# Kernel optimization log

Hardware: AMD Instinct MI355X
Metric: run time of the kernel (lower is better)

Reference implementation:

```python
import jax, jax.numpy as jnp
import numpy as np

B, L, C, Y, DIM = 64, 64, 4, 0, 2  # batch, lattice size, n_colors, tau-shift, shift axis


def _coloring_probes():
    # k x k block coloring for C colors (C must be a perfect square here; C=4 -> k=2)
    k = int(round(np.sqrt(C)))
    i = np.arange(L)[:, None]
    j = np.arange(L)[None, :]
    col = (i % k) * k + (j % k)  # (L, L) color index per site
    probes = (col[None, :, :] == np.arange(C)[:, None, None]).astype(np.float32)
    return jnp.asarray(probes)  # (C, L, L) one-hot color masks


def _gelu(x):
    return jax.nn.gelu(x, approximate=False)  # torch nn.GELU default = exact erf


def _forward(x, sW1, sb1, sW2, sb2, sW3, sb3, aW1, ab1, aW2, ab2):
    # site features: phi, 2D lattice laplacian (periodic), phi_{x+tau}, phi_{x-tau}
    lap = (jnp.roll(x, 1, 1) + jnp.roll(x, -1, 1)
           + jnp.roll(x, 1, 2) + jnp.roll(x, -1, 2) - 4.0 * x)
    phi_tau = jnp.roll(x, -Y, axis=DIM)
    phi_mtau = jnp.roll(x, Y, axis=DIM)
    f = jnp.stack([x, lap, phi_tau, phi_mtau], axis=-1)  # (B, L, L, 4)
    h = _gelu(f @ sW1 + sb1)
    h = _gelu(h @ sW2 + sb2)
    h = (h @ sW3 + sb3)[..., 0]                          # (B, L, L)
    h_mean = h.mean(axis=(1, 2))
    h_var = jnp.var(h, axis=(1, 2), ddof=1)              # torch .var() is unbiased
    h_sq_mean = (h * h).mean(axis=(1, 2))
    a = jnp.stack([h_mean, h_var, h_sq_mean], axis=1)    # (B, 3)
    a = _gelu(a @ aW1 + ab1)
    return (a @ aW2 + ab2)[..., 0]                       # (B,)


def setup_inputs() -> dict:
    key = jax.random.key(0)
    ks = jax.random.split(key, 8)

    def w(k, shape, fan_in):
        return jax.random.normal(k, shape, jnp.float32) / np.sqrt(fan_in).astype(np.float32)

    return {
        "x": jax.random.normal(ks[0], (B, L, L), jnp.float32),
        "signs": jax.random.randint(ks[1], (C, B, L, L), 0, 2, jnp.int32),
        "site_W1": w(ks[2], (4, 128), 4),
        "site_b1": jnp.zeros((128,), jnp.float32),
        "site_W2": w(ks[3], (128, 128), 128),
        "site_b2": jnp.zeros((128,), jnp.float32),
        "site_W3": w(ks[4], (128, 1), 128),
        "site_b3": jnp.zeros((1,), jnp.float32),
        "agg_W1": w(ks[5], (3, 64), 3),
        "agg_b1": jnp.zeros((64,), jnp.float32),
        "agg_W2": w(ks[6], (64, 1), 64),
        "agg_b2": jnp.zeros((1,), jnp.float32),
    }


def reference(x, signs, site_W1, site_b1, site_W2, site_b2, site_W3, site_b3,
              agg_W1, agg_b1, agg_W2, agg_b2):
    params = (site_W1, site_b1, site_W2, site_b2, site_W3, site_b3,
              agg_W1, agg_b1, agg_W2, agg_b2)
    fsum = lambda xx: _forward(xx, *params).sum()  # batches are independent, so sum is safe

    # first-order gradient grad_x F, shape (B, L, L)
    grad = jax.grad(fsum)(x)

    # probing laplacian with coloring + Rademacher signs, batched over colors
    probes = _coloring_probes()                                   # (C, L, L)
    z = (2.0 * signs.astype(jnp.float32) - 1.0) * probes[:, None]  # (C, B, L, L)
    # hvp_c = H @ z_c via forward-over-reverse AD (replaces per-color autograd.grad loop)
    hvp = jax.vmap(lambda zc: jax.jvp(jax.grad(fsum), (x,), (zc,))[1])(z)  # (C, B, L, L)
    lapl = jnp.sum(hvp * z, axis=(0, 2, 3))                       # (B,)

    # pack (grad, lapl) into one array: (B, L*L + 1)
    return jnp.concatenate([grad.reshape(B, -1), lapl[:, None]], axis=1)
```

## Files before the change

### kernel.cpp

```cpp
#include <hip/hip_runtime.h>
#include <hip/hip_bf16.h>
#include <math.h>

typedef unsigned short ushort_t;
typedef unsigned int   u32;
typedef __attribute__((ext_vector_type(8))) short s8v;
typedef __attribute__((ext_vector_type(4))) float f4v;
typedef __attribute__((ext_vector_type(2))) float f2v;

#define LL 64
#define NB 64
#define NSITE 4096
#define BN 262144
#define RED_OFF 0
#define WA_OFF  11264
#define WB_OFF  11392
#define PL_OFF  12288
#define BF_OFF  (PL_OFF + 6*BN)

#if __has_builtin(__builtin_amdgcn_exp2f)
#define EXP2F(x) __builtin_amdgcn_exp2f(x)
#else
#define EXP2F(x) __expf(0.6931471805599453f*(x))
#endif

__device__ __forceinline__ void gelu3(float u, float &h, float &d, float &e){
  float E   = __expf(-0.5f * u * u);
  float phi = 0.3989422804014327f * E;
  float az  = fabsf(u) * 0.70710678118654752f;
  float t   = __builtin_amdgcn_rcpf(1.0f + 0.3275911f * az);
  float p   = t*(0.254829592f + t*(-0.284496736f + t*(1.421413741f + t*(-1.453152027f + t*1.061405429f))));
  float erfabs = 1.0f - p * E;
  float erfv   = __builtin_copysignf(erfabs, u);
  float Phi = 0.5f * (1.0f + erfv);
  h = u * Phi;
  d = Phi + u * phi;
  e = phi * (2.0f - u * u);
}

__device__ __forceinline__ void gelu3x2(f2v u, f2v &h, f2v &d, f2v &e){
  f2v u2 = u * u;
  f2v m  = u2 * (-0.72134752044448170368f);
  f2v E;  E.x = EXP2F(m.x); E.y = EXP2F(m.y);
  f2v phi = 0.3989422804014327f * E;
  f2v az;
  az.x = fabsf(u.x) * 0.70710678118654752f;
  az.y = fabsf(u.y) * 0.70710678118654752f;
  f2v den = 0.3275911f * az + 1.0f;
  f2v t;  t.x = __builtin_amdgcn_rcpf(den.x); t.y = __builtin_amdgcn_rcpf(den.y);
  f2v p = t*(0.254829592f + t*(-0.284496736f + t*(1.421413741f + t*(-1.453152027f + t*1.061405429f))));
  f2v erfabs = 1.0f - p * E;
  f2v erfv;
  erfv.x = __builtin_copysignf(erfabs.x, u.x);
  erfv.y = __builtin_copysignf(erfabs.y, u.y);
  f2v Phi = 0.5f * erfv + 0.5f;
  h = u * Phi;
  d = u * phi + Phi;
  e = phi * (2.0f - u2);
}

#define DPP_ADD(v, ctrl) { \
  int _si = __builtin_amdgcn_update_dpp(0, __builtin_bit_cast(int, v), ctrl, 0xf, 0xf, true); \
  v += __builtin_bit_cast(float, _si); }

__device__ __forceinline__ float redjb16(float v){
  DPP_ADD(v, 0xB1);
  DPP_ADD(v, 0x4E);
  DPP_ADD(v, 0x124);
  DPP_ADD(v, 0x128);
  return v;
}
__device__ __forceinline__ float red64(float v){
  v = redjb16(v);
  v += __shfl_xor(v, 16);
  v += __shfl_xor(v, 32);
  return v;
}

__device__ __forceinline__ ushort_t bf16rne(float v){
  union { float f; u32 i; } x; x.f = v;
  u32 r = x.i + 0x7FFFu + ((x.i >> 16) & 1u);
  return (ushort_t)(r >> 16);
}
__device__ __forceinline__ u32 pkbf(float a, float b){
  __hip_bfloat162 t = __float22bfloat162_rn(make_float2(a, b));
  u32 r;
  __builtin_memcpy(&r, &t, sizeof(r));
  return r;
}
__device__ __forceinline__ u32 pkbf2(f2v v){
  return pkbf(v.x, v.y);
}

__global__ __launch_bounds__(256, 4) void k_pre(
    const float* __restrict__ W1g, const float* __restrict__ W2g,
    float* __restrict__ ws, float* __restrict__ out)
{
  int t = blockIdx.x * 256 + threadIdx.x;
  if (blockIdx.x == 0 && threadIdx.x < 128) {
    int k = threadIdx.x;
    ws[WA_OFF + k] = W1g[k] + W1g[256+k] + W1g[384+k];
    ws[WB_OFF + k] = W1g[128+k];
  }
  if (blockIdx.x == 1 && threadIdx.x < 64) {
    out[(size_t)threadIdx.x*4097 + 4096] = 0.f;
  }
  short* BF = (short*)(ws + BF_OFF);
  int w = t >> 9, nt = (t >> 8) & 1, kt = (t >> 6) & 3, lane = t & 63;
  int q = lane >> 4, nlo = lane & 15;
  int n = w*32 + nt*16 + nlo;
  s8v vh;
  #pragma unroll
  for (int jj = 0; jj < 8; ++jj) {
    int k = kt*32 + q*8 + jj;
    vh[jj] = (short)bf16rne(W2g[k*128 + n]);
  }
  *(s8v*)&BF[t*8] = vh;
}

__global__ __launch_bounds__(256, 3) void k_c1(
    const float* __restrict__ xg, const int* __restrict__ signs,
    const float* __restrict__ b1g, const float* __restrict__ b2g,
    const float* __restrict__ W3g, const float* __restrict__ b3g,
    float* __restrict__ ws)
{
  __shared__ alignas(16) short AF[12288];
  __shared__ float xS[6][64];
  __shared__ char  zS[6][64];
  __shared__ float EP[16][7][4];

  const int tid  = threadIdx.x;
  const int lane = tid & 63;
  const int w    = tid >> 6;
  const int rg4  = (lane >> 4) << 2;

  const int blk = blockIdx.x;
  const int b   = blk >> 4;
  const int i0  = (blk & 15) << 2;

  const s8v* BhT = (const s8v*)((const short*)(ws + BF_OFF)) + (w*512 + lane);

  float4 b2H[2], w3H[2];
  #pragma unroll
  for (int nt = 0; nt < 2; ++nt) {
    int n0 = w*32 + nt*16 + rg4;
    b2H[nt] = *(const float4*)(b2g + n0);
    w3H[nt] = *(const float4*)(W3g + n0);
  }
  float b3v = b3g[0];

  const int s_  = tid & 15;
  const int ko_ = tid >> 4;
  float4 waH[2], wbH[2], b1H[2];
  #pragma unroll
  for (int half = 0; half < 2; ++half) {
    int k0 = ko_*8 + half*4;
    waH[half] = *(const float4*)(ws + WA_OFF + k0);
    wbH[half] = *(const float4*)(ws + WB_OFF + k0);
    b1H[half] = *(const float4*)(b1g + k0);
  }

  for (int t = tid; t < 384; t += 256) {
    int r = t >> 6, j = t & 63;
    int gr = (i0 - 1 + r) & 63;
    xS[r][j] = xg[(size_t)b*NSITE + gr*64 + j];
    int c = ((gr & 1) << 1) | (j & 1);
    zS[r][j] = (char)(2*signs[((c*NB + b)*LL + gr)*LL + j] - 1);
  }
  __syncthreads();

  float racc[10];
  #pragma unroll
  for (int n = 0; n < 10; ++n) racc[n] = 0.f;

  const f4v Zf = {0.f, 0.f, 0.f, 0.f};

  #pragma unroll 1
  for (int ch = 0; ch < 16; ++ch) {
    const int lr = 1 + (ch >> 2);
    const int jb = ch & 3;
    const int i  = i0 + (ch >> 2);

    s8v pb00 = BhT[0],  pb10 = BhT[256];
    s8v pb01 = BhT[64], pb11 = BhT[320];

    {
      int j = jb*16 + s_, jm = (j+63)&63, jp = (j+1)&63;
      float p = xS[lr][j];
      float l = xS[lr-1][j] + xS[lr+1][j] + xS[lr][jm] + xS[lr][jp] - 4.0f*p;
      u32 vv[6][4];
      #pragma unroll
      for (int half = 0; half < 2; ++half) {
        const float* waA = (const float*)&waH[half];
        const float* wbA = (const float*)&wbH[half];
        const float* b1A = (const float*)&b1H[half];
        #pragma unroll
        for (int pr = 0; pr < 2; ++pr) {
          f2v wa = {waA[pr*2], waA[pr*2+1]};
          f2v wb = {wbA[pr*2], wbA[pr*2+1]};
          f2v bb = {b1A[pr*2], b1A[pr*2+1]};
          f2v u = p*wa + l*wb + bb;
          f2v h, dd, ee;
          gelu3x2(u, h, dd, ee);
          int c = half*2 + pr;
          vv[0][c] = pkbf2(h);
          vv[1][c] = pkbf2(dd*wa);
          vv[2][c] = pkbf2(dd*wb);
          f2v ea = ee*wa, eb = ee*wb;
          vv[3][c] = pkbf2(ea*wa);
          vv[4][c] = pkbf2(ea*wb);
          vv[5][c] = pkbf2(eb*wb);
        }
      }
      short* base = &AF[(ko_>>2)*3072 + ((ko_&3)*16 + s_)*8];
      #pragma unroll
      for (int pp = 0; pp < 6; ++pp)
        *(int4*)&base[pp*512] = make_int4((int)vv[pp][0], (int)vv[pp][1],
                                          (int)vv[pp][2], (int)vv[pp][3]);
    }
    __syncthreads();

    f4v acc[6][2];
    __builtin_amdgcn_s_setprio(1);
    {
      const short* base = &AF[lane*8];
      #pragma unroll
      for (int pp = 0; pp < 6; ++pp) {
        s8v ah = *(const s8v*)&base[pp*512];
        acc[pp][0] = __builtin_amdgcn_mfma_f32_16x16x32_bf16(pb00, ah, Zf, 0, 0, 0);
        acc[pp][1] = __builtin_amdgcn_mfma_f32_16x16x32_bf16(pb10, ah, Zf, 0, 0, 0);
      }
    }
    s8v bh0 = pb01, bh1 = pb11;
    #pragma unroll 1
    for (int kt = 1; kt < 4; ++kt) {
      s8v nh0 = bh0, nh1 = bh1;
      if (kt != 3) {
        int o = (kt + 1) * 64;
        nh0 = BhT[o]; nh1 = BhT[256 + o];
      }
      const short* base = &AF[kt*3072 + lane*8];
      #pragma unroll
      for (int pp = 0; pp < 6; ++pp) {
        s8v ah = *(const s8v*)&base[pp*512];
        acc[pp][0] = __builtin_amdgcn_mfma_f32_16x16x32_bf16(bh0, ah, acc[pp][0], 0, 0, 0);
        acc[pp][1] = __builtin_amdgcn_mfma_f32_16x16x32_bf16(bh1, ah, acc[pp][1], 0, 0, 0);
      }
      bh0 = nh0; bh1 = nh1;
    }
    __builtin_amdgcn_s_setprio(0);

    {
      f2v qh = {0.f,0.f}, qA = {0.f,0.f}, qB = {0.f,0.f};
      f2v qa = {0.f,0.f}, qb = {0.f,0.f}, qc = {0.f,0.f};
      #pragma unroll
      for (int nt = 0; nt < 2; ++nt) {
        const float* b2A = (const float*)&b2H[nt];
        const float* w3A = (const float*)&w3H[nt];
        #pragma unroll
        for (int pr = 0; pr < 2; ++pr) {
          const int r0 = pr*2;
          f2v uu  = (f2v){acc[0][nt][r0], acc[0][nt][r0+1]}
                  + (f2v){b2A[r0], b2A[r0+1]};
          f2v w3p = {w3A[r0], w3A[r0+1]};
          f2v h2, d2, e2;
          gelu3x2(uu, h2, d2, e2);
          f2v wd = w3p*d2, we = w3p*e2;
          f2v A  = {acc[1][nt][r0], acc[1][nt][r0+1]};
          f2v Bv = {acc[2][nt][r0], acc[2][nt][r0+1]};
          f2v t3 = {acc[3][nt][r0], acc[3][nt][r0+1]};
          f2v t4 = {acc[4][nt][r0], acc[4][nt][r0+1]};
          f2v t5 = {acc[5][nt][r0], acc[5][nt][r0+1]};
          qh += w3p*h2;
          qA += wd*A;
          qB += wd*Bv;
          qa += we*(A*A)   + wd*t3;
          qb += we*(A*Bv)  + wd*t4;
          qc += we*(Bv*Bv) + wd*t5;
        }
      }
      float sh = qh.x + qh.y;
      float sA = qA.x + qA.y;
      float sB = qB.x + qB.y;
      float sa = qa.x + qa.y;
      float sb = qb.x + qb.y;
      float sc = qc.x + qc.y;
      sh += __shfl_xor(sh, 16); sh += __shfl_xor(sh, 32);
      sA += __shfl_xor(sA, 16); sA += __shfl_xor(sA, 32);
      sB += __shfl_xor(sB, 16); sB += __shfl_xor(sB, 32);
      sa += __shfl_xor(sa, 16); sa += __shfl_xor(sa, 32);
      sb += __shfl_xor(sb, 16); sb += __shfl_xor(sb, 32);
      sc += __shfl_xor(sc, 16); sc += __shfl_xor(sc, 32);
      if (lane < 16) {
        EP[lane][0][w] = sh;
        EP[lane][1][w] = sA;
        EP[lane][2][w] = sB;
        EP[lane][3][w] = sa;
        EP[lane][4][w] = sb;
        EP[lane][5][w] = sc;
      }
    }
    __syncthreads();

    if (tid < 16) {
      int s = tid;
      float h = 0.f, RA = 0.f, RB = 0.f, TAa = 0.f, TAb = 0.f, TBb = 0.f;
      #pragma unroll
      for (int ww = 0; ww < 4; ++ww) {
        h   += EP[s][0][ww];
        RA  += EP[s][1][ww];
        RB  += EP[s][2][ww];
        TAa += EP[s][3][ww];
        TAb += EP[s][4][ww];
        TBb += EP[s][5][ww];
      }
      h += b3v;
      float* P = ws + PL_OFF;
      int j = jb*16 + s;
      size_t site = (size_t)b*NSITE + i*64 + j;
      P[0*BN + site] = h;
      P[1*BN + site] = RA;
      P[2*BN + site] = RB;
      P[3*BN + site] = TAa;
      P[4*BN + site] = TAb;
      P[5*BN + site] = TBb;

      int jm = (j+63)&63, jp = (j+1)&63;
      int c0 = ((i & 1) << 1) | (j & 1);
      float hd[4] = {0.f, 0.f, 0.f, 0.f};
      hd[c0]     = (float)zS[lr][j] * (RA - 4.0f*RB);
      hd[c0 ^ 1] = (float)(zS[lr][jm] + zS[lr][jp]) * RB;
      hd[c0 ^ 2] = (float)(zS[lr-1][j] + zS[lr+1][j]) * RB;
      racc[0] += h;
      racc[1] += h*h;
      #pragma unroll
      for (int cc = 0; cc < 4; ++cc) {
        racc[2+cc] += hd[cc];
        racc[6+cc] += h*hd[cc];
      }
    }
  }

  if (tid < 16) {
    #pragma unroll
    for (int n = 0; n < 10; ++n) racc[n] = redjb16(racc[n]);
    if (tid == 0) {
      #pragma unroll
      for (int n = 0; n < 10; ++n) ws[RED_OFF + blk*10 + n] = racc[n];
    }
  }
}

__global__ __launch_bounds__(256, 4) void k_c2(
    const int* __restrict__ signs,
    const float* __restrict__ aW1g, const float* __restrict__ ab1g,
    const float* __restrict__ aW2g,
    float* __restrict__ ws, float* __restrict__ out)
{
  __shared__ float part[4];
  __shared__ float coefL[10];
  __shared__ float redS[10];
  __shared__ float cbS[6][64];
  int blk = blockIdx.x;
  int b = blk >> 4, rg = blk & 15;
  int tid = threadIdx.x;

  if (tid < 160) {
    int qq = tid >> 4, g = tid & 15;
    float v = ws[RED_OFF + (b*16 + g)*10 + qq];
    v = redjb16(v);
    if (g == 0) redS[qq] = v;
  }
  __syncthreads();

  if (tid < 64) {
    int k = tid;
    const float Nf = 4096.0f, Nm1 = 4095.0f;
    float S1 = redS[0], S2 = redS[1];
    float m = S1/Nf, q = S2/Nf;
    float v = (S2 - S1*S1/Nf)/Nm1;
    float w0 = aW1g[k], w1 = aW1g[64+k], w2 = aW1g[128+k];
    float t = m*w0 + v*w1 + q*w2 + ab1g[k];
    float gh, gd, ge;
    gelu3(t, gh, gd, ge);
    float o = aW2g[k];
    float g1o = gd*o, g2o = ge*o;
    float da0 = w0*g1o, da1 = w1*g1o, da2 = w2*g1o;
    float M00 = w0*w0*g2o, M01 = w0*w1*g2o, M02 = w0*w2*g2o;
    float M11 = w1*w1*g2o, M12 = w1*w2*g2o, M22 = w2*w2*g2o;
    da0 = red64(da0); da1 = red64(da1); da2 = red64(da2);
    M00 = red64(M00); M01 = red64(M01); M02 = red64(M02);
    M11 = red64(M11); M12 = red64(M12); M22 = red64(M22);
    if (k == 0) {
      coefL[0] = da0/Nf - 2.0f*da1*m/Nm1;
      coefL[1] = 2.0f*da1/Nm1 + 2.0f*da2/Nf;
      #pragma unroll
      for (int c = 0; c < 4; ++c) {
        float s1 = redS[2 + c], s2 = redS[6 + c];
        float md = s1/Nf, qd = 2.0f*s2/Nf;
        float vd = (2.0f*s2 - 2.0f*S1*s1/Nf)/Nm1;
        float dd0 = M00*md + M01*vd + M02*qd;
        float dd1 = M01*md + M11*vd + M12*qd;
        float dd2 = M02*md + M12*vd + M22*qd;
        coefL[2+c] = dd0/Nf - 2.0f*(dd1*m + da1*md)/Nm1;
        coefL[6+c] = 2.0f*dd1/Nm1 + 2.0f*dd2/Nf;
      }
    }
  }
  __syncthreads();

  const float* P = ws + PL_OFF;
  int base = b*NSITE;
  float alpha = coefL[0], beta = coefL[1];

  for (int t = tid; t < 384; t += 256) {
    int r = t >> 6, jj = t & 63;
    int gr = (rg*4 - 1 + r) & 63;
    int sidx = base + gr*64 + jj;
    cbS[r][jj] = (alpha + beta*P[sidx]) * P[2*BN + sidx];
  }
  __syncthreads();

  int rl = tid >> 6, j = tid & 63;
  int i = rg*4 + rl;
  int im=(i+63)&63, ip=(i+1)&63, jm=(j+63)&63, jp=(j+1)&63;
  int s  = base + i*64 + j;
  float h  = P[s], RA = P[BN+s], RB = P[2*BN+s];
  float TAa= P[3*BN+s], TAb = P[4*BN+s], TBb = P[5*BN+s];
  float g  = alpha + beta*h;
  int lr2 = rl + 1;
  float cb  = cbS[lr2][j];
  float cbu = cbS[lr2-1][j], cbd = cbS[lr2+1][j];
  float cbl = cbS[lr2][jm],  cbr = cbS[lr2][jp];
  float grad = g*RA + (cbu + cbd + cbl + cbr - 4.0f*cb);
  out[(size_t)b*4097 + i*64 + j] = grad;

  int c0 = ((i & 1) << 1) | (j & 1);
  int c1 = c0 ^ 1, c2 = c0 ^ 2;
  float zv = 2.0f*(float)signs[((c0*NB + b)*LL + i )*LL + j ] - 1.0f;
  float zl = 2.0f*(float)signs[((c1*NB + b)*LL + i )*LL + jm] - 1.0f;
  float zr = 2.0f*(float)signs[((c1*NB + b)*LL + i )*LL + jp] - 1.0f;
  float zu = 2.0f*(float)signs[((c2*NB + b)*LL + im)*LL + j ] - 1.0f;
  float zd = 2.0f*(float)signs[((c2*NB + b)*LL + ip)*LL + j ] - 1.0f;
  float sjr = zl + zr, sud = zu + zd;
  float hd0 = zv*(RA - 4.0f*RB);
  float hd1 = sjr*RB, hd2 = sud*RB;
  float gd0 = coefL[2+c0] + coefL[6+c0]*h + beta*hd0;
  float gd1 = coefL[2+c1] + coefL[6+c1]*h + beta*hd1;
  float gd2 = coefL[2+c2] + coefL[6+c2]*h + beta*hd2;
  float ca0 = gd0*RA + g*( zv*TAa - 4.0f*zv*TAb );
  float cb0 = gd0*RB + g*( zv*TAb - 4.0f*zv*TBb );
  float cb1 = gd1*RB + g*( sjr*TBb );
  float cb2 = gd2*RB + g*( sud*TBb );
  float contrib = zv*ca0 - 4.0f*zv*cb0 + sjr*cb1 + sud*cb2;

  float vsum = red64(contrib);
  int wv = tid >> 6;
  if ((tid & 63) == 0) part[wv] = vsum;
  __syncthreads();
  if (tid == 0)
    atomicAdd(out + (size_t)b*4097 + 4096,
              part[0] + part[1] + part[2] + part[3]);
}

extern "C" void kernel_launch(void* const* d_in, const int* in_sizes, int n_in,
                              void* d_out, int out_size, void* d_ws, size_t ws_size,
                              hipStream_t stream) {
  const float* xg    = (const float*)d_in[0];
  const int*   signs = (const int*)d_in[1];
  const float* W1    = (const float*)d_in[2];
  const float* b1    = (const float*)d_in[3];
  const float* W2    = (const float*)d_in[4];
  const float* b2    = (const float*)d_in[5];
  const float* W3    = (const float*)d_in[6];
  const float* b3    = (const float*)d_in[7];
  const float* aW1   = (const float*)d_in[8];
  const float* ab1   = (const float*)d_in[9];
  const float* aW2   = (const float*)d_in[10];
  float* ws  = (float*)d_ws;
  float* out = (float*)d_out;

  hipLaunchKernelGGL(k_pre, dim3(8),    dim3(256), 0, stream, W1, W2, ws, out);
  hipLaunchKernelGGL(k_c1,  dim3(1024), dim3(256), 0, stream,
                     xg, signs, b1, b2, W3, b3, ws);
  hipLaunchKernelGGL(k_c2,  dim3(1024), dim3(256), 0, stream,
                     signs, aW1, ab1, aW2, ws, out);
}
```

Baseline: 181.2 us.

## Fuse second pass into main kernel via last-block-per-batch atomic ticket

Removes the separate k_c2 launch. Each k_c1 block increments a per-batch counter after writing its partial reductions, and the last of the 16 blocks for a batch runs the aggregation and writes the whole 4096-site gradient and Laplacian. This saves one kernel launch and the global sync between kernels, and drops the output atomicAdd. In exchange the per-batch epilogue is serialized on one block (64 blocks doing 4096 sites each) instead of spread over 1024 blocks, which can leave a long tail.

```diff
diff --git a/kernel.cpp b/kernel.cpp
--- a/kernel.cpp
+++ b/kernel.cpp
@@ -13,6 +13,7 @@
 #define NSITE 4096
 #define BN 262144
 #define RED_OFF 0
+#define CNT_OFF 10240
 #define WA_OFF  11264
 #define WB_OFF  11392
 #define PL_OFF  12288
@@ -94,7 +95,7 @@
 
 __global__ __launch_bounds__(256, 4) void k_pre(
     const float* __restrict__ W1g, const float* __restrict__ W2g,
-    float* __restrict__ ws, float* __restrict__ out)
+    float* __restrict__ ws)
 {
   int t = blockIdx.x * 256 + threadIdx.x;
   if (blockIdx.x == 0 && threadIdx.x < 128) {
@@ -103,7 +104,7 @@
     ws[WB_OFF + k] = W1g[128+k];
   }
   if (blockIdx.x == 1 && threadIdx.x < 64) {
-    out[(size_t)threadIdx.x*4097 + 4096] = 0.f;
+    ((int*)ws)[CNT_OFF + threadIdx.x] = 0;
   }
   short* BF = (short*)(ws + BF_OFF);
   int w = t >> 9, nt = (t >> 8) & 1, kt = (t >> 6) & 3, lane = t & 63;
@@ -122,12 +123,18 @@
     const float* __restrict__ xg, const int* __restrict__ signs,
     const float* __restrict__ b1g, const float* __restrict__ b2g,
     const float* __restrict__ W3g, const float* __restrict__ b3g,
-    float* __restrict__ ws)
+    const float* __restrict__ aW1g, const float* __restrict__ ab1g,
+    const float* __restrict__ aW2g,
+    float* __restrict__ ws, float* __restrict__ out)
 {
   __shared__ alignas(16) short AF[12288];
   __shared__ float xS[6][64];
   __shared__ char  zS[6][64];
   __shared__ float EP[16][7][4];
+  __shared__ float coefL[10];
+  __shared__ float redS[10];
+  __shared__ float partS[4];
+  __shared__ int   tickS;
 
   const int tid  = threadIdx.x;
   const int lane = tid & 63;
@@ -349,21 +356,13 @@
       for (int n = 0; n < 10; ++n) ws[RED_OFF + blk*10 + n] = racc[n];
     }
   }
-}
-
-__global__ __launch_bounds__(256, 4) void k_c2(
-    const int* __restrict__ signs,
-    const float* __restrict__ aW1g, const float* __restrict__ ab1g,
-    const float* __restrict__ aW2g,
-    float* __restrict__ ws, float* __restrict__ out)
-{
-  __shared__ float part[4];
-  __shared__ float coefL[10];
-  __shared__ float redS[10];
-  __shared__ float cbS[6][64];
-  int blk = blockIdx.x;
-  int b = blk >> 4, rg = blk & 15;
-  int tid = threadIdx.x;
+
+  __threadfence();
+  __syncthreads();
+  if (tid == 0) tickS = atomicAdd(((int*)ws) + CNT_OFF + b, 1);
+  __syncthreads();
+  if (tickS != 15) return;
+  __threadfence();
 
   if (tid < 160) {
     int qq = tid >> 4, g = tid & 15;
@@ -410,57 +409,56 @@
   __syncthreads();
 
   const float* P = ws + PL_OFF;
-  int base = b*NSITE;
-  float alpha = coefL[0], beta = coefL[1];
-
-  for (int t = tid; t < 384; t += 256) {
-    int r = t >> 6, jj = t & 63;
-    int gr = (rg*4 - 1 + r) & 63;
-    int sidx = base + gr*64 + jj;
-    cbS[r][jj] = (alpha + beta*P[sidx]) * P[2*BN + sidx];
-  }
-  __syncthreads();
-
-  int rl = tid >> 6, j = tid & 63;
-  int i = rg*4 + rl;
-  int im=(i+63)&63, ip=(i+1)&63, jm=(j+63)&63, jp=(j+1)&63;
-  int s  = base + i*64 + j;
-  float h  = P[s], RA = P[BN+s], RB = P[2*BN+s];
-  float TAa= P[3*BN+s], TAb = P[4*BN+s], TBb = P[5*BN+s];
-  float g  = alpha + beta*h;
-  int lr2 = rl + 1;
-  float cb  = cbS[lr2][j];
-  float cbu = cbS[lr2-1][j], cbd = cbS[lr2+1][j];
-  float cbl = cbS[lr2][jm],  cbr = cbS[lr2][jp];
-  float grad = g*RA + (cbu + cbd + cbl + cbr - 4.0f*cb);
-  out[(size_t)b*4097 + i*64 + j] = grad;
-
-  int c0 = ((i & 1) << 1) | (j & 1);
-  int c1 = c0 ^ 1, c2 = c0 ^ 2;
-  float zv = 2.0f*(float)signs[((c0*NB + b)*LL + i )*LL + j ] - 1.0f;
-  float zl = 2.0f*(float)signs[((c1*NB + b)*LL + i )*LL + jm] - 1.0f;
-  float zr = 2.0f*(float)signs[((c1*NB + b)*LL + i )*LL + jp] - 1.0f;
-  float zu = 2.0f*(float)signs[((c2*NB + b)*LL + im)*LL + j ] - 1.0f;
-  float zd = 2.0f*(float)signs[((c2*NB + b)*LL + ip)*LL + j ] - 1.0f;
-  float sjr = zl + zr, sud = zu + zd;
-  float hd0 = zv*(RA - 4.0f*RB);
-  float hd1 = sjr*RB, hd2 = sud*RB;
-  float gd0 = coefL[2+c0] + coefL[6+c0]*h + beta*hd0;
-  float gd1 = coefL[2+c1] + coefL[6+c1]*h + beta*hd1;
-  float gd2 = coefL[2+c2] + coefL[6+c2]*h + beta*hd2;
-  float ca0 = gd0*RA + g*( zv*TAa - 4.0f*zv*TAb );
-  float cb0 = gd0*RB + g*( zv*TAb - 4.0f*zv*TBb );
-  float cb1 = gd1*RB + g*( sjr*TBb );
-  float cb2 = gd2*RB + g*( sud*TBb );
-  float contrib = zv*ca0 - 4.0f*zv*cb0 + sjr*cb1 + sud*cb2;
-
-  float vsum = red64(contrib);
-  int wv = tid >> 6;
-  if ((tid & 63) == 0) part[wv] = vsum;
+  const int base = b*NSITE;
+  const float alpha = coefL[0], beta = coefL[1];
+
+  float* cbF = (float*)AF;
+  #pragma unroll 1
+  for (int s = tid; s < 4096; s += 256) {
+    cbF[s] = (alpha + beta*P[base + s]) * P[2*BN + base + s];
+  }
+  __syncthreads();
+
+  float lacc = 0.f;
+  #pragma unroll 1
+  for (int s = tid; s < 4096; s += 256) {
+    int i = s >> 6, j = s & 63;
+    int im=(i+63)&63, ip=(i+1)&63, jm=(j+63)&63, jp=(j+1)&63;
+    int gidx = base + s;
+    float h  = P[gidx], RA = P[BN+gidx], RB = P[2*BN+gidx];
+    float TAa= P[3*BN+gidx], TAb = P[4*BN+gidx], TBb = P[5*BN+gidx];
+    float g  = alpha + beta*h;
+    float cb  = cbF[s];
+    float cbu = cbF[im*64+j], cbd = cbF[ip*64+j];
+    float cbl = cbF[i*64+jm], cbr = cbF[i*64+jp];
+    float grad = g*RA + (cbu + cbd + cbl + cbr - 4.0f*cb);
+    out[(size_t)b*4097 + s] = grad;
+
+    int c0 = ((i & 1) << 1) | (j & 1);
+    int c1 = c0 ^ 1, c2 = c0 ^ 2;
+    float zv = 2.0f*(float)signs[((c0*NB + b)*LL + i )*LL + j ] - 1.0f;
+    float zl = 2.0f*(float)signs[((c1*NB + b)*LL + i )*LL + jm] - 1.0f;
+    float zr = 2.0f*(float)signs[((c1*NB + b)*LL + i )*LL + jp] - 1.0f;
+    float zu = 2.0f*(float)signs[((c2*NB + b)*LL + im)*LL + j ] - 1.0f;
+    float zd = 2.0f*(float)signs[((c2*NB + b)*LL + ip)*LL + j ] - 1.0f;
+    float sjr = zl + zr, sud = zu + zd;
+    float hd0 = zv*(RA - 4.0f*RB);
+    float hd1 = sjr*RB, hd2 = sud*RB;
+    float gd0 = coefL[2+c0] + coefL[6+c0]*h + beta*hd0;
+    float gd1 = coefL[2+c1] + coefL[6+c1]*h + beta*hd1;
+    float gd2 = coefL[2+c2] + coefL[6+c2]*h + beta*hd2;
+    float ca0 = gd0*RA + g*( zv*TAa - 4.0f*zv*TAb );
+    float cb0 = gd0*RB + g*( zv*TAb - 4.0f*zv*TBb );
+    float cb1 = gd1*RB + g*( sjr*TBb );
+    float cb2 = gd2*RB + g*( sud*TBb );
+    lacc += zv*ca0 - 4.0f*zv*cb0 + sjr*cb1 + sud*cb2;
+  }
+
+  float vsum = red64(lacc);
+  if ((tid & 63) == 0) partS[tid >> 6] = vsum;
   __syncthreads();
   if (tid == 0)
-    atomicAdd(out + (size_t)b*4097 + 4096,
-              part[0] + part[1] + part[2] + part[3]);
+    out[(size_t)b*4097 + 4096] = partS[0] + partS[1] + partS[2] + partS[3];
 }
 
 extern "C" void kernel_launch(void* const* d_in, const int* in_sizes, int n_in,
@@ -480,9 +478,7 @@
   float* ws  = (float*)d_ws;
   float* out = (float*)d_out;
 
-  hipLaunchKernelGGL(k_pre, dim3(8),    dim3(256), 0, stream, W1, W2, ws, out);
+  hipLaunchKernelGGL(k_pre, dim3(8),    dim3(256), 0, stream, W1, W2, ws);
   hipLaunchKernelGGL(k_c1,  dim3(1024), dim3(256), 0, stream,
-                     xg, signs, b1, b2, W3, b3, ws);
-  hipLaunchKernelGGL(k_c2,  dim3(1024), dim3(256), 0, stream,
-                     signs, aW1, ab1, aW2, ws, out);
-}
+                     xg, signs, b1, b2, W3, b3, aW1, ab1, aW2, ws, out);
+}
```

Result: slower. 294.2 us (+62.4%).
